# Kernel tuning notes

Measured on AMD Instinct MI355X. Metric: run time of the kernel, lower is better.

Reference implementation:

```python
import jax, jax.numpy as jnp
import numpy as np

SCALING = 2.0  # lora_alpha / r


def setup_inputs() -> dict:
    key = jax.random.key(0)
    ks = jax.random.split(key, 6)
    B, S, D_IN, D_OUT, R = 4, 4096, 4096, 4096, 32
    x = jax.random.normal(ks[0], (B, S, D_IN), dtype=jnp.float32)
    W = jax.random.normal(ks[1], (D_OUT, D_IN), dtype=jnp.float32) * 0.02
    b = jax.random.normal(ks[2], (D_OUT,), dtype=jnp.float32) * 0.02
    A = jax.random.normal(ks[3], (R, D_IN), dtype=jnp.float32) * 0.02
    B_w = jax.random.normal(ks[4], (D_OUT, R), dtype=jnp.float32) * 0.02
    # per-sample activation offsets, in [1, S]
    alora_offsets = jax.random.randint(ks[5], (B,), 1, S + 1, dtype=jnp.int32)
    return {"x": x, "alora_offsets": alora_offsets, "W": W, "b": b, "A": A, "B_w": B_w}


def reference(x, alora_offsets, W, b, A, B_w):
    # base linear: y = x @ W^T + b
    base = jnp.einsum("bsd,od->bso", x, W) + b  # [B, S, D_OUT]
    # LoRA path on full sequence (dropout is identity at inference, p=0)
    lora = jnp.einsum("bsr,or->bso", jnp.einsum("bsd,rd->bsr", x, A), B_w) * SCALING
    # per-sample tail mask: only last k = min(offset, S) positions get the LoRA update
    S = x.shape[1]
    k = jnp.minimum(alora_offsets, S)  # [B]
    pos = jnp.arange(S, dtype=jnp.int32)
    mask = pos[None, :] >= (S - k)[:, None]  # [B, S] True on the tail
    return base + jnp.where(mask[:, :, None], lora, jnp.zeros((), base.dtype))
```

## Files before the change

kernel.cpp:

```cpp
#include <hip/hip_runtime.h>
#include <hip/hip_bf16.h>

typedef __attribute__((ext_vector_type(8))) short short8;
typedef __attribute__((ext_vector_type(4))) float f32x4;

#define GLOAD_LDS16(gp, lp)                                                      \
  __builtin_amdgcn_global_load_lds(                                              \
      (const __attribute__((address_space(1))) void*)(gp),                       \
      (__attribute__((address_space(3))) void*)(lp), 16, 0, 0)

#define SBAR() asm volatile("s_barrier" ::: "memory")
#define VMC(n)                                                                   \
  do {                                                                           \
    asm volatile("s_waitcnt vmcnt(" #n ")" ::: "memory");                        \
    __builtin_amdgcn_sched_barrier(0);                                           \
  } while (0)

__device__ __forceinline__ unsigned short f2bf_rne(float f) {
  union { float f; unsigned int u; } v; v.f = f;
  unsigned int u = v.u;
  u += 0x7fffu + ((u >> 16) & 1u);
  return (unsigned short)(u >> 16);
}

__global__ void cvt_f32_bf16(const float* __restrict__ src,
                             unsigned short* __restrict__ dst, int n8) {
  int i = blockIdx.x * blockDim.x + threadIdx.x;
  int stride = gridDim.x * blockDim.x;
  const f32x4* s4 = (const f32x4*)src;
  short8* d8 = (short8*)dst;
  for (; i < n8; i += stride) {
    f32x4 a = s4[2 * i], b = s4[2 * i + 1];
    short8 o;
    o[0] = (short)f2bf_rne(a[0]); o[1] = (short)f2bf_rne(a[1]);
    o[2] = (short)f2bf_rne(a[2]); o[3] = (short)f2bf_rne(a[3]);
    o[4] = (short)f2bf_rne(b[0]); o[5] = (short)f2bf_rne(b[1]);
    o[6] = (short)f2bf_rne(b[2]); o[7] = (short)f2bf_rne(b[3]);
    d8[i] = o;
  }
}

__global__ __launch_bounds__(256) void lora_t_kernel(
    const unsigned short* __restrict__ xb,
    const unsigned short* __restrict__ Ab,
    const int* __restrict__ offs,
    unsigned short* __restrict__ T)
{
  __shared__ unsigned short xs[64 * 64];
  __shared__ unsigned short as_[32 * 64];
  const int t = threadIdx.x;
  const int m0 = blockIdx.x * 64;
  const int l = t & 63, w = t >> 6;
  const int lr = l & 15, lk = (l >> 4) * 8;
  const int arow = t >> 3, acol = (t & 7) * 8;
  f32x4 acc0 = {0, 0, 0, 0}, acc1 = {0, 0, 0, 0};
  for (int kt = 0; kt < 64; ++kt) {
    __syncthreads();
    const int kof = kt * 64 + acol;
    GLOAD_LDS16(xb + (size_t)(m0 + arow) * 4096 + kof,      (char*)xs + (arow * 64 + acol) * 2);
    GLOAD_LDS16(xb + (size_t)(m0 + 32 + arow) * 4096 + kof, (char*)xs + ((32 + arow) * 64 + acol) * 2);
    GLOAD_LDS16(Ab + (size_t)arow * 4096 + kof,             (char*)as_ + (arow * 64 + acol) * 2);
    __syncthreads();
#pragma unroll
    for (int kk = 0; kk < 2; ++kk) {
      short8 a  = *(const short8*)&xs[(w * 16 + lr) * 64 + kk * 32 + lk];
      short8 b0 = *(const short8*)&as_[lr * 64 + kk * 32 + lk];
      short8 b1 = *(const short8*)&as_[(16 + lr) * 64 + kk * 32 + lk];
      acc0 = __builtin_amdgcn_mfma_f32_16x16x32_bf16(a, b0, acc0, 0, 0, 0);
      acc1 = __builtin_amdgcn_mfma_f32_16x16x32_bf16(a, b1, acc1, 0, 0, 0);
    }
  }
  const int rowb = (l >> 4) * 4;
#pragma unroll
  for (int j = 0; j < 4; ++j) {
    int m = m0 + w * 16 + rowb + j;
    int bb = m >> 12, s = m & 4095;
    int kcut = offs[bb]; if (kcut > 4096) kcut = 4096;
    bool keep = s >= 4096 - kcut;
    T[(size_t)m * 32 + lr]      = keep ? f2bf_rne(2.0f * acc0[j]) : (unsigned short)0;
    T[(size_t)m * 32 + 16 + lr] = keep ? f2bf_rne(2.0f * acc1[j]) : (unsigned short)0;
  }
}

__global__ __launch_bounds__(512, 2) void gemm_kernel(
    const unsigned short* __restrict__ xb,
    const unsigned short* __restrict__ Wb,
    const unsigned short* __restrict__ Tm,
    const unsigned short* __restrict__ Bwb,
    const float* __restrict__ bias,
    float* __restrict__ out)
{
  constexpr int K = 4096;
  extern __shared__ char smem[];

  const int bid = blockIdx.x;
  const int swz = (bid & 7) * 128 + (bid >> 3);
  const int m0 = (swz >> 4) * 256;
  const int n0 = (swz & 15) * 256;

  const int t = threadIdx.x;
  const int l = t & 63, w = t >> 6;
  const int wqr = w >> 2;
  const int pr = (w >> 1) & 1;
  const int pc = w & 1;
  const int lr = l & 15, hi = l >> 4;
  const int e0 = (hi ^ (lr & 7)) * 8;

  const int srow = t >> 3;
  const int schunk = ((t & 7) ^ ((t >> 3) & 7)) * 8;
  const unsigned short* pA0 = xb + (size_t)(m0 + srow) * K + schunk;
  const unsigned short* pA1 = xb + (size_t)(m0 + 128 + srow) * K + schunk;
  const unsigned short* pB0 = Wb + (size_t)(n0 + srow) * K + schunk;
  const unsigned short* pB1 = Wb + (size_t)(n0 + 128 + srow) * K + schunk;
  unsigned short* sm = (unsigned short*)smem;
  const int ldst = t * 16;

#define STG(PTR, SLOT, ISB, HALF, KT)                                           \
  do {                                                                          \
    const unsigned short* g_ = (PTR) + (KT) * 64;                               \
    char* d_ = smem + (SLOT) * 65536 + (ISB) * 32768 + (HALF) * 16384 + ldst;   \
    GLOAD_LDS16(g_, d_);                                                        \
    GLOAD_LDS16(g_ + (size_t)64 * K, d_ + 8192);                                \
  } while (0)

  f32x4 acc[2][4][4];
  short8 afr[4];

  {
    const unsigned short* tp = Tm + (size_t)(m0 + wqr * 128 + pr * 64 + lr) * 32 + hi * 8;
    short8 la[4];
#pragma unroll
    for (int i = 0; i < 4; ++i) la[i] = *(const short8*)(tp + i * 512);
    short8 lb[2][4];
#pragma unroll
    for (int qc = 0; qc < 2; ++qc)
#pragma unroll
      for (int j = 0; j < 4; ++j)
        lb[qc][j] = *(const short8*)(Bwb + (size_t)(n0 + qc * 128 + pc * 64 + j * 16 + lr) * 32 + hi * 8);
#pragma unroll
    for (int qc = 0; qc < 2; ++qc)
#pragma unroll
      for (int i = 0; i < 4; ++i)
#pragma unroll
        for (int j = 0; j < 4; ++j)
          acc[qc][i][j] = __builtin_amdgcn_mfma_f32_16x16x32_bf16(
              la[i], lb[qc][j], (f32x4){0.f, 0.f, 0.f, 0.f}, 0, 0, 0);
  }

  STG(pB1, 0, 1, 1, 0);
  STG(pA0, 0, 0, 0, 0);
  STG(pA1, 0, 0, 1, 0);
  STG(pB0, 0, 1, 0, 0);
  STG(pB0, 1, 1, 0, 1);
  VMC(2);
  SBAR();

#define PHASE(SLOT, QC, KK, READA, STG_STMT, WAIT_STMT)                         \
  {                                                                             \
    const unsigned short* Ah = sm + (SLOT) * 32768 + wqr * 8192;                \
    const unsigned short* Bh = sm + (SLOT) * 32768 + 16384 + (QC) * 8192;       \
    const int ek = e0 ^ ((KK) * 32);                                            \
    if (READA) {                                                                \
      _Pragma("unroll")                                                         \
      for (int i = 0; i < 4; ++i)                                               \
        afr[i] = *(const short8*)(Ah + (pr * 64 + i * 16 + lr) * 64 + ek);      \
    }                                                                           \
    short8 bfr[4];                                                              \
    _Pragma("unroll")                                                           \
    for (int j = 0; j < 4; ++j)                                                 \
      bfr[j] = *(const short8*)(Bh + (pc * 64 + j * 16 + lr) * 64 + ek);        \
    STG_STMT;                                                                   \
    SBAR();                                                                     \
    __builtin_amdgcn_s_setprio(1);                                              \
    _Pragma("unroll")                                                           \
    for (int i = 0; i < 4; ++i)                                                 \
      _Pragma("unroll")                                                         \
      for (int j = 0; j < 4; ++j)                                               \
        acc[QC][i][j] = __builtin_amdgcn_mfma_f32_16x16x32_bf16(                \
            afr[i], bfr[j], acc[QC][i][j], 0, 0, 0);                            \
    __builtin_amdgcn_s_setprio(0);                                              \
    WAIT_STMT;                                                                  \
    SBAR();                                                                     \
  }

  for (int I = 0; I < 31; ++I) {
    const int a = 2 * I;
    PHASE(0, 0, 0, 1, STG(pB1, 1, 1, 1, a + 1), ((void)0));
    PHASE(0, 1, 0, 0, STG(pA0, 1, 0, 0, a + 1), ((void)0));
    PHASE(0, 0, 1, 1, STG(pA1, 1, 0, 1, a + 1), ((void)0));
    PHASE(0, 1, 1, 0, STG(pB0, 0, 1, 0, a + 2), VMC(2));
    PHASE(1, 0, 0, 1, STG(pB1, 0, 1, 1, a + 2), ((void)0));
    PHASE(1, 1, 0, 0, STG(pA0, 0, 0, 0, a + 2), ((void)0));
    PHASE(1, 0, 1, 1, STG(pA1, 0, 0, 1, a + 2), ((void)0));
    PHASE(1, 1, 1, 0, STG(pB0, 1, 1, 0, a + 3), VMC(2));
  }
  PHASE(0, 0, 0, 1, STG(pB1, 1, 1, 1, 63), ((void)0));
  PHASE(0, 1, 0, 0, STG(pA0, 1, 0, 0, 63), ((void)0));
  PHASE(0, 0, 1, 1, STG(pA1, 1, 0, 1, 63), ((void)0));
  PHASE(0, 1, 1, 0, ((void)0), VMC(0));
  PHASE(1, 0, 0, 1, ((void)0), ((void)0));
  PHASE(1, 1, 0, 0, ((void)0), ((void)0));
  PHASE(1, 0, 1, 1, ((void)0), ((void)0));
  PHASE(1, 1, 1, 0, ((void)0), ((void)0));
#undef PHASE
#undef STG

  float bv[2][4];
#pragma unroll
  for (int qc = 0; qc < 2; ++qc)
#pragma unroll
    for (int j = 0; j < 4; ++j)
      bv[qc][j] = bias[n0 + qc * 128 + pc * 64 + j * 16 + lr];
  const int rowb = hi * 4;
#pragma unroll
  for (int qc = 0; qc < 2; ++qc)
#pragma unroll
    for (int i = 0; i < 4; ++i)
#pragma unroll
      for (int e = 0; e < 4; ++e) {
        int row = m0 + wqr * 128 + pr * 64 + i * 16 + rowb + e;
        float* orow = out + (size_t)row * 4096 + n0 + qc * 128 + pc * 64;
#pragma unroll
        for (int j = 0; j < 4; ++j) orow[j * 16 + lr] = acc[qc][i][j][e] + bv[qc][j];
      }
}

extern "C" void kernel_launch(void* const* d_in, const int* in_sizes, int n_in,
                              void* d_out, int out_size, void* d_ws, size_t ws_size,
                              hipStream_t stream) {
  const float* x   = (const float*)d_in[0];
  const int* offs  = (const int*)d_in[1];
  const float* W   = (const float*)d_in[2];
  const float* b   = (const float*)d_in[3];
  const float* A   = (const float*)d_in[4];
  const float* Bw  = (const float*)d_in[5];
  float* out = (float*)d_out;

  char* ws = (char*)d_ws;
  unsigned short* xb  = (unsigned short*)ws;
  unsigned short* Wb  = (unsigned short*)(ws + 134217728);
  unsigned short* Ab  = (unsigned short*)(ws + 167772160);
  unsigned short* Bwb = (unsigned short*)(ws + 168034304);
  unsigned short* T   = (unsigned short*)(ws + 168296448);

  hipFuncSetAttribute((const void*)gemm_kernel,
                      hipFuncAttributeMaxDynamicSharedMemorySize, 131072);

  cvt_f32_bf16<<<2048, 256, 0, stream>>>(x, xb, 67108864 / 8);
  cvt_f32_bf16<<<2048, 256, 0, stream>>>(W, Wb, 16777216 / 8);
  cvt_f32_bf16<<<64, 256, 0, stream>>>(A, Ab, 131072 / 8);
  cvt_f32_bf16<<<64, 256, 0, stream>>>(Bw, Bwb, 131072 / 8);
  lora_t_kernel<<<256, 256, 0, stream>>>(xb, Ab, offs, T);
  gemm_kernel<<<1024, 512, 131072, stream>>>(xb, Wb, T, Bwb, b, out);
}
```

Before: 608.2 us.

## Fuse x bf16 conversion into LoRA down-projection kernel and convert B in-GEMM

The separate fp32-to-bf16 conversion of x is folded into the LoRA T kernel. That kernel now reads fp32 x, packs it to bf16, writes xb for the main GEMM and stages the tile in padded LDS for the MFMA. A is converted on the fly the same way, and B_w is converted inside the GEMM prologue, which removes three launches and one extra read of x. The risk is that the fused kernel runs on only 256 blocks with synchronous loads and no prefetch, so the conversion of the large x tensor may become latency-bound on fewer waves than the old 2048-block conversion.

```diff
diff --git a/kernel.cpp b/kernel.cpp
--- a/kernel.cpp
+++ b/kernel.cpp
@@ -21,6 +21,15 @@
   unsigned int u = v.u;
   u += 0x7fffu + ((u >> 16) & 1u);
   return (unsigned short)(u >> 16);
+}
+
+__device__ __forceinline__ short8 pack8(f32x4 a, f32x4 b) {
+  short8 o;
+  o[0] = (short)f2bf_rne(a[0]); o[1] = (short)f2bf_rne(a[1]);
+  o[2] = (short)f2bf_rne(a[2]); o[3] = (short)f2bf_rne(a[3]);
+  o[4] = (short)f2bf_rne(b[0]); o[5] = (short)f2bf_rne(b[1]);
+  o[6] = (short)f2bf_rne(b[2]); o[7] = (short)f2bf_rne(b[3]);
+  return o;
 }
 
 __global__ void cvt_f32_bf16(const float* __restrict__ src,
@@ -30,24 +39,19 @@
   const f32x4* s4 = (const f32x4*)src;
   short8* d8 = (short8*)dst;
   for (; i < n8; i += stride) {
-    f32x4 a = s4[2 * i], b = s4[2 * i + 1];
-    short8 o;
-    o[0] = (short)f2bf_rne(a[0]); o[1] = (short)f2bf_rne(a[1]);
-    o[2] = (short)f2bf_rne(a[2]); o[3] = (short)f2bf_rne(a[3]);
-    o[4] = (short)f2bf_rne(b[0]); o[5] = (short)f2bf_rne(b[1]);
-    o[6] = (short)f2bf_rne(b[2]); o[7] = (short)f2bf_rne(b[3]);
-    d8[i] = o;
-  }
-}
-
-__global__ __launch_bounds__(256) void lora_t_kernel(
-    const unsigned short* __restrict__ xb,
-    const unsigned short* __restrict__ Ab,
+    d8[i] = pack8(s4[2 * i], s4[2 * i + 1]);
+  }
+}
+
+__global__ __launch_bounds__(256) void cvt_lora_kernel(
+    const float* __restrict__ x,
+    const float* __restrict__ A,
     const int* __restrict__ offs,
+    unsigned short* __restrict__ xb,
     unsigned short* __restrict__ T)
 {
-  __shared__ unsigned short xs[64 * 64];
-  __shared__ unsigned short as_[32 * 64];
+  __shared__ unsigned short xs[64 * 72];
+  __shared__ unsigned short as_[32 * 72];
   const int t = threadIdx.x;
   const int m0 = blockIdx.x * 64;
   const int l = t & 63, w = t >> 6;
@@ -55,17 +59,25 @@
   const int arow = t >> 3, acol = (t & 7) * 8;
   f32x4 acc0 = {0, 0, 0, 0}, acc1 = {0, 0, 0, 0};
   for (int kt = 0; kt < 64; ++kt) {
+    const int kof = kt * 64 + acol;
+    const float* px0 = x + (size_t)(m0 + arow) * 4096 + kof;
+    const float* px1 = x + (size_t)(m0 + 32 + arow) * 4096 + kof;
+    const float* pa  = A + (size_t)arow * 4096 + kof;
+    short8 s0 = pack8(*(const f32x4*)px0, *(const f32x4*)(px0 + 4));
+    short8 s1 = pack8(*(const f32x4*)px1, *(const f32x4*)(px1 + 4));
+    short8 sa = pack8(*(const f32x4*)pa,  *(const f32x4*)(pa + 4));
+    *(short8*)(xb + (size_t)(m0 + arow) * 4096 + kof)      = s0;
+    *(short8*)(xb + (size_t)(m0 + 32 + arow) * 4096 + kof) = s1;
     __syncthreads();
-    const int kof = kt * 64 + acol;
-    GLOAD_LDS16(xb + (size_t)(m0 + arow) * 4096 + kof,      (char*)xs + (arow * 64 + acol) * 2);
-    GLOAD_LDS16(xb + (size_t)(m0 + 32 + arow) * 4096 + kof, (char*)xs + ((32 + arow) * 64 + acol) * 2);
-    GLOAD_LDS16(Ab + (size_t)arow * 4096 + kof,             (char*)as_ + (arow * 64 + acol) * 2);
+    *(short8*)&xs[arow * 72 + acol]        = s0;
+    *(short8*)&xs[(32 + arow) * 72 + acol] = s1;
+    *(short8*)&as_[arow * 72 + acol]       = sa;
     __syncthreads();
 #pragma unroll
     for (int kk = 0; kk < 2; ++kk) {
-      short8 a  = *(const short8*)&xs[(w * 16 + lr) * 64 + kk * 32 + lk];
-      short8 b0 = *(const short8*)&as_[lr * 64 + kk * 32 + lk];
-      short8 b1 = *(const short8*)&as_[(16 + lr) * 64 + kk * 32 + lk];
+      short8 a  = *(const short8*)&xs[(w * 16 + lr) * 72 + kk * 32 + lk];
+      short8 b0 = *(const short8*)&as_[lr * 72 + kk * 32 + lk];
+      short8 b1 = *(const short8*)&as_[(16 + lr) * 72 + kk * 32 + lk];
       acc0 = __builtin_amdgcn_mfma_f32_16x16x32_bf16(a, b0, acc0, 0, 0, 0);
       acc1 = __builtin_amdgcn_mfma_f32_16x16x32_bf16(a, b1, acc1, 0, 0, 0);
     }
@@ -86,7 +98,7 @@
     const unsigned short* __restrict__ xb,
     const unsigned short* __restrict__ Wb,
     const unsigned short* __restrict__ Tm,
-    const unsigned short* __restrict__ Bwb,
+    const float* __restrict__ Bw,
     const float* __restrict__ bias,
     float* __restrict__ out)
 {
@@ -135,8 +147,10 @@
 #pragma unroll
     for (int qc = 0; qc < 2; ++qc)
 #pragma unroll
-      for (int j = 0; j < 4; ++j)
-        lb[qc][j] = *(const short8*)(Bwb + (size_t)(n0 + qc * 128 + pc * 64 + j * 16 + lr) * 32 + hi * 8);
+      for (int j = 0; j < 4; ++j) {
+        const float* bp = Bw + (size_t)(n0 + qc * 128 + pc * 64 + j * 16 + lr) * 32 + hi * 8;
+        lb[qc][j] = pack8(*(const f32x4*)bp, *(const f32x4*)(bp + 4));
+      }
 #pragma unroll
     for (int qc = 0; qc < 2; ++qc)
 #pragma unroll
@@ -237,19 +251,14 @@
   float* out = (float*)d_out;
 
   char* ws = (char*)d_ws;
-  unsigned short* xb  = (unsigned short*)ws;
-  unsigned short* Wb  = (unsigned short*)(ws + 134217728);
-  unsigned short* Ab  = (unsigned short*)(ws + 167772160);
-  unsigned short* Bwb = (unsigned short*)(ws + 168034304);
-  unsigned short* T   = (unsigned short*)(ws + 168296448);
+  unsigned short* xb = (unsigned short*)ws;
+  unsigned short* Wb = (unsigned short*)(ws + 134217728);
+  unsigned short* T  = (unsigned short*)(ws + 167772160);
 
   hipFuncSetAttribute((const void*)gemm_kernel,
                       hipFuncAttributeMaxDynamicSharedMemorySize, 131072);
 
-  cvt_f32_bf16<<<2048, 256, 0, stream>>>(x, xb, 67108864 / 8);
+  cvt_lora_kernel<<<256, 256, 0, stream>>>(x, A, offs, xb, T);
   cvt_f32_bf16<<<2048, 256, 0, stream>>>(W, Wb, 16777216 / 8);
-  cvt_f32_bf16<<<64, 256, 0, stream>>>(A, Ab, 131072 / 8);
-  cvt_f32_bf16<<<64, 256, 0, stream>>>(Bw, Bwb, 131072 / 8);
-  lora_t_kernel<<<256, 256, 0, stream>>>(xb, Ab, offs, T);
-  gemm_kernel<<<1024, 512, 131072, stream>>>(xb, Wb, T, Bwb, b, out);
-}
+  gemm_kernel<<<1024, 512, 131072, stream>>>(xb, Wb, T, Bw, b, out);
+}
```

Result: no change. 615.1 us (+1.1%).

## Fuse x/W/A fp32-to-bf16 conversion into the LoRA down-projection kernel

Applied to the files above, without the earlier changes.

Replaces the separate conversion kernels for x, W and A plus the LoRA T kernel with a single kernel. It reads fp32 x and A directly, converts them in registers, writes bf16 x out for the main GEMM and stages the tiles in padded LDS for the MFMA. W conversion is appended to the tail of each block. The aim is to drop a full re-read of bf16 x and several launches. In exchange, each block is smaller (32 rows), loads are synchronous instead of async LDS loads, and A is reconverted in every block.

```diff
diff --git a/kernel.cpp b/kernel.cpp
--- a/kernel.cpp
+++ b/kernel.cpp
@@ -21,6 +21,15 @@
   unsigned int u = v.u;
   u += 0x7fffu + ((u >> 16) & 1u);
   return (unsigned short)(u >> 16);
+}
+
+__device__ __forceinline__ short8 pack8(f32x4 a, f32x4 b) {
+  short8 o;
+  o[0] = (short)f2bf_rne(a[0]); o[1] = (short)f2bf_rne(a[1]);
+  o[2] = (short)f2bf_rne(a[2]); o[3] = (short)f2bf_rne(a[3]);
+  o[4] = (short)f2bf_rne(b[0]); o[5] = (short)f2bf_rne(b[1]);
+  o[6] = (short)f2bf_rne(b[2]); o[7] = (short)f2bf_rne(b[3]);
+  return o;
 }
 
 __global__ void cvt_f32_bf16(const float* __restrict__ src,
@@ -30,55 +39,62 @@
   const f32x4* s4 = (const f32x4*)src;
   short8* d8 = (short8*)dst;
   for (; i < n8; i += stride) {
-    f32x4 a = s4[2 * i], b = s4[2 * i + 1];
-    short8 o;
-    o[0] = (short)f2bf_rne(a[0]); o[1] = (short)f2bf_rne(a[1]);
-    o[2] = (short)f2bf_rne(a[2]); o[3] = (short)f2bf_rne(a[3]);
-    o[4] = (short)f2bf_rne(b[0]); o[5] = (short)f2bf_rne(b[1]);
-    o[6] = (short)f2bf_rne(b[2]); o[7] = (short)f2bf_rne(b[3]);
-    d8[i] = o;
-  }
-}
-
-__global__ __launch_bounds__(256) void lora_t_kernel(
-    const unsigned short* __restrict__ xb,
-    const unsigned short* __restrict__ Ab,
+    d8[i] = pack8(s4[2 * i], s4[2 * i + 1]);
+  }
+}
+
+__global__ __launch_bounds__(256) void cvt_lora_kernel(
+    const float* __restrict__ x,
+    const float* __restrict__ A,
+    const float* __restrict__ W,
     const int* __restrict__ offs,
+    unsigned short* __restrict__ xb,
+    unsigned short* __restrict__ Wb,
     unsigned short* __restrict__ T)
 {
-  __shared__ unsigned short xs[64 * 64];
-  __shared__ unsigned short as_[32 * 64];
+  __shared__ unsigned short xs[32 * 72];
+  __shared__ unsigned short as_[32 * 72];
   const int t = threadIdx.x;
-  const int m0 = blockIdx.x * 64;
+  const int m0 = blockIdx.x * 32;
   const int l = t & 63, w = t >> 6;
+  const int wr = w >> 1, wc = w & 1;
   const int lr = l & 15, lk = (l >> 4) * 8;
   const int arow = t >> 3, acol = (t & 7) * 8;
-  f32x4 acc0 = {0, 0, 0, 0}, acc1 = {0, 0, 0, 0};
+  f32x4 acc = {0, 0, 0, 0};
   for (int kt = 0; kt < 64; ++kt) {
+    const int kof = kt * 64 + acol;
+    const float* px = x + (size_t)(m0 + arow) * 4096 + kof;
+    const float* pa = A + (size_t)arow * 4096 + kof;
+    short8 s0 = pack8(*(const f32x4*)px, *(const f32x4*)(px + 4));
+    short8 sa = pack8(*(const f32x4*)pa, *(const f32x4*)(pa + 4));
+    *(short8*)(xb + (size_t)(m0 + arow) * 4096 + kof) = s0;
     __syncthreads();
-    const int kof = kt * 64 + acol;
-    GLOAD_LDS16(xb + (size_t)(m0 + arow) * 4096 + kof,      (char*)xs + (arow * 64 + acol) * 2);
-    GLOAD_LDS16(xb + (size_t)(m0 + 32 + arow) * 4096 + kof, (char*)xs + ((32 + arow) * 64 + acol) * 2);
-    GLOAD_LDS16(Ab + (size_t)arow * 4096 + kof,             (char*)as_ + (arow * 64 + acol) * 2);
+    *(short8*)&xs[arow * 72 + acol]  = s0;
+    *(short8*)&as_[arow * 72 + acol] = sa;
     __syncthreads();
 #pragma unroll
     for (int kk = 0; kk < 2; ++kk) {
-      short8 a  = *(const short8*)&xs[(w * 16 + lr) * 64 + kk * 32 + lk];
-      short8 b0 = *(const short8*)&as_[lr * 64 + kk * 32 + lk];
-      short8 b1 = *(const short8*)&as_[(16 + lr) * 64 + kk * 32 + lk];
-      acc0 = __builtin_amdgcn_mfma_f32_16x16x32_bf16(a, b0, acc0, 0, 0, 0);
-      acc1 = __builtin_amdgcn_mfma_f32_16x16x32_bf16(a, b1, acc1, 0, 0, 0);
+      short8 a = *(const short8*)&xs[(wr * 16 + lr) * 72 + kk * 32 + lk];
+      short8 b = *(const short8*)&as_[(wc * 16 + lr) * 72 + kk * 32 + lk];
+      acc = __builtin_amdgcn_mfma_f32_16x16x32_bf16(a, b, acc, 0, 0, 0);
     }
   }
   const int rowb = (l >> 4) * 4;
 #pragma unroll
   for (int j = 0; j < 4; ++j) {
-    int m = m0 + w * 16 + rowb + j;
+    int m = m0 + wr * 16 + rowb + j;
     int bb = m >> 12, s = m & 4095;
     int kcut = offs[bb]; if (kcut > 4096) kcut = 4096;
     bool keep = s >= 4096 - kcut;
-    T[(size_t)m * 32 + lr]      = keep ? f2bf_rne(2.0f * acc0[j]) : (unsigned short)0;
-    T[(size_t)m * 32 + 16 + lr] = keep ? f2bf_rne(2.0f * acc1[j]) : (unsigned short)0;
+    T[(size_t)m * 32 + wc * 16 + lr] = keep ? f2bf_rne(2.0f * acc[j]) : (unsigned short)0;
+  }
+  const f32x4* s4 = (const f32x4*)W;
+  short8* d8 = (short8*)Wb;
+  const int base = blockIdx.x * 4096;
+#pragma unroll
+  for (int q = 0; q < 16; ++q) {
+    int idx = base + q * 256 + t;
+    d8[idx] = pack8(s4[2 * idx], s4[2 * idx + 1]);
   }
 }
 
@@ -239,17 +255,13 @@
   char* ws = (char*)d_ws;
   unsigned short* xb  = (unsigned short*)ws;
   unsigned short* Wb  = (unsigned short*)(ws + 134217728);
-  unsigned short* Ab  = (unsigned short*)(ws + 167772160);
-  unsigned short* Bwb = (unsigned short*)(ws + 168034304);
-  unsigned short* T   = (unsigned short*)(ws + 168296448);
+  unsigned short* Bwb = (unsigned short*)(ws + 167772160);
+  unsigned short* T   = (unsigned short*)(ws + 168034304);
 
   hipFuncSetAttribute((const void*)gemm_kernel,
                       hipFuncAttributeMaxDynamicSharedMemorySize, 131072);
 
-  cvt_f32_bf16<<<2048, 256, 0, stream>>>(x, xb, 67108864 / 8);
-  cvt_f32_bf16<<<2048, 256, 0, stream>>>(W, Wb, 16777216 / 8);
-  cvt_f32_bf16<<<64, 256, 0, stream>>>(A, Ab, 131072 / 8);
   cvt_f32_bf16<<<64, 256, 0, stream>>>(Bw, Bwb, 131072 / 8);
-  lora_t_kernel<<<256, 256, 0, stream>>>(xb, Ab, offs, T);
+  cvt_lora_kernel<<<512, 256, 0, stream>>>(x, A, W, offs, xb, Wb, T);
   gemm_kernel<<<1024, 512, 131072, stream>>>(xb, Wb, T, Bwb, b, out);
 }
```

New measurement: 581.4 us. 1.05x faster.
